# Kernel optimization log

Hardware: AMD Instinct MI355X
Metric: run time of the kernel (lower is better)

## Reference

```python
import jax, jax.numpy as jnp
import numpy as np
from jax import lax

EPS = 1e-4  # BatchNorm eps from the module
K = 3       # kernel_size
PAD = 1     # padding


def setup_inputs() -> dict:
    key = jax.random.key(0)
    k1, k2, k3 = jax.random.split(key, 3)
    N, Cin, H, Wd = 32, 256, 56, 56
    Cout = 256
    x = jax.random.normal(k1, (N, Cin, H, Wd), dtype=jnp.float32)
    gamma = jnp.ones((Cin,), dtype=jnp.float32)
    beta_bn = jnp.zeros((Cin,), dtype=jnp.float32)
    W = jax.random.normal(k2, (Cout, Cin, K, K), dtype=jnp.float32) * 0.05
    b = jax.random.normal(k3, (Cout,), dtype=jnp.float32) * 0.01
    return {"x": x, "gamma": gamma, "beta_bn": beta_bn, "W": W, "b": b}


def _conv(x, w, padding):
    return lax.conv_general_dilated(
        x, w, window_strides=(1, 1),
        padding=[(padding, padding), (padding, padding)],
        dimension_numbers=("NCHW", "OIHW", "NCHW"))


def reference(x, gamma, beta_bn, W, b):
    # BatchNorm2d in training mode: batch statistics over (N, H, W), biased var
    mu = jnp.mean(x, axis=(0, 2, 3), keepdims=True)
    var = jnp.var(x, axis=(0, 2, 3), keepdims=True)
    xn = (x - mu) * lax.rsqrt(var + EPS)
    xn = xn * gamma[None, :, None, None] + beta_bn[None, :, None, None]

    # BinActiv: per-pixel channel-mean of |x|, then sign-binarize
    m = jnp.mean(jnp.abs(xn), axis=1, keepdims=True)  # [N,1,H,W]
    xb = jnp.sign(xn)

    # Binarize weights; alpha = L1 norm per output filter / n
    n = W.shape[1] * W.shape[2] * W.shape[3]
    alpha = jnp.sum(jnp.abs(W), axis=(1, 2, 3)) / n  # [Cout]
    Wb = jnp.sign(W)

    y = _conv(xb, Wb, PAD) + b[None, :, None, None]

    # beta map: box filter (stride 1) over channel-mean magnitudes
    box = jnp.full((1, 1, K, K), 1.0 / (K * K), dtype=x.dtype)
    beta_map = _conv(m, box, PAD)  # [N,1,Ho,Wo]

    out = jax.nn.relu(y * beta_map * alpha[None, :, None, None])
    return out
```

## Files before the change

### kernel.cpp

```cpp
#include <hip/hip_runtime.h>
#include <cstdint>
#include <cstddef>

#define N_    32
#define C_    256
#define H_    56
#define W_    56
#define HW_   (H_ * W_)
#define NHW_  (N_ * HW_)
#define COUT_ 256
#define EPS_  1e-4f
#define PW_   58
#define PIMG_ (PW_ * PW_)

__global__ void k_bn_partial(const float* __restrict__ x,
                             float* __restrict__ ps, float* __restrict__ pq) {
    const int c = blockIdx.x >> 3;
    const int s = blockIdx.x & 7;
    const int t = threadIdx.x;
    float sm = 0.f, sq = 0.f;
    for (int n = s * 4; n < s * 4 + 4; ++n) {
        const float4* p = (const float4*)(x + (size_t)(n * C_ + c) * HW_);
        for (int i = t; i < HW_ / 4; i += 256) {
            float4 v = p[i];
            sm += v.x + v.y + v.z + v.w;
            sq += v.x * v.x + v.y * v.y + v.z * v.z + v.w * v.w;
        }
    }
    __shared__ float ls[256], lq[256];
    ls[t] = sm; lq[t] = sq;
    __syncthreads();
    for (int off = 128; off >= 1; off >>= 1) {
        if (t < off) { ls[t] += ls[t + off]; lq[t] += lq[t + off]; }
        __syncthreads();
    }
    if (t == 0) { ps[s * C_ + c] = ls[0]; pq[s * C_ + c] = lq[0]; }
}

__global__ void k_bn_final(const float* __restrict__ ps, const float* __restrict__ pq,
                           const float* __restrict__ gamma, const float* __restrict__ beta,
                           float* __restrict__ a, float* __restrict__ bb) {
    const int c = threadIdx.x;
    float sm = 0.f, sq = 0.f;
    for (int s = 0; s < 8; ++s) { sm += ps[s * C_ + c]; sq += pq[s * C_ + c]; }
    float mu   = sm * (1.f / NHW_);
    float var  = sq * (1.f / NHW_) - mu * mu;
    float rstd = rsqrtf(var + EPS_);
    float g    = gamma[c] * rstd;
    a[c]  = g;
    bb[c] = beta[c] - mu * g;
}

__global__ void k_wpack(const float* __restrict__ Wt, float* __restrict__ alpha,
                        uint64_t* __restrict__ wbits, int* __restrict__ ctab) {
    const int co = blockIdx.x;
    const int ci = threadIdx.x;
    const int lane = ci & 63, wave = ci >> 6;
    const float* p = Wt + (size_t)(co * C_ + ci) * 9;
    float wv[9];
    float asum = 0.f;
#pragma unroll
    for (int t = 0; t < 9; ++t) { wv[t] = p[t]; asum += fabsf(wv[t]); }
    __shared__ int Pl[9];
    if (ci < 9) Pl[ci] = 0;
    __syncthreads();
#pragma unroll
    for (int t = 0; t < 9; ++t) {
        uint64_t mask = __ballot(wv[t] > 0.f);
        if (lane == 0) {
            wbits[(co * 9 + t) * 4 + wave] = mask;
            atomicAdd(&Pl[t], (int)__popcll(mask));
        }
    }
    __shared__ float red[256];
    red[ci] = asum;
    __syncthreads();
    for (int off = 128; off >= 1; off >>= 1) {
        if (ci < off) red[ci] += red[ci + off];
        __syncthreads();
    }
    if (ci == 0) alpha[co] = red[0] * (1.f / 2304.f);
    if (ci < 9) {
        const int rc = ci / 3, cc = ci % 3;
        unsigned m9 = (rc == 0 ? 0x007u : 0u) | (rc == 2 ? 0x1C0u : 0u)
                    | (cc == 0 ? 0x049u : 0u) | (cc == 2 ? 0x124u : 0u);
        int s = 0;
#pragma unroll
        for (int t = 0; t < 9; ++t)
            if ((m9 >> t) & 1) s += 2 * Pl[t] - 256;
        ctab[ci * 256 + co] = s;
    }
}

__global__ void k_mpack(const float* __restrict__ x, const float* __restrict__ a,
                        const float* __restrict__ bb, uint64_t* __restrict__ xbits,
                        float* __restrict__ m) {
    const int p = blockIdx.x * 256 + threadIdx.x;
    const int wd = blockIdx.y;
    const int n = p / HW_;
    const int hw = p - n * HW_;
    const int h = hw / W_;
    const int w = hw - h * W_;
    const float* xp = x + (size_t)n * C_ * HW_ + (size_t)(wd * 64) * HW_ + hw;
    float macc = 0.f;
    uint64_t bw = 0;
#pragma unroll
    for (int j = 0; j < 64; ++j) {
        const int c = wd * 64 + j;
        float xn = fmaf(xp[(size_t)j * HW_], a[c], bb[c]);
        macc += fabsf(xn);
        bw |= (xn > 0.f) ? (1ull << j) : 0ull;
    }
    xbits[((size_t)n * PIMG_ + (size_t)(h + 1) * PW_ + (w + 1)) * 4 + wd] = bw;
    atomicAdd(&m[p], macc * (1.f / C_));
}

__global__ void k_box(const float* __restrict__ m, float* __restrict__ beta_map) {
    const int idx = blockIdx.x * 256 + threadIdx.x;
    if (idx >= NHW_) return;
    const int w = idx % W_;
    const int h = (idx / W_) % H_;
    const int n = idx / HW_;
    const float* mp = m + (size_t)n * HW_;
    float s = 0.f;
#pragma unroll
    for (int dh = 0; dh < 3; ++dh) {
        int ih = h + dh - 1;
        if (ih < 0 || ih >= H_) continue;
#pragma unroll
        for (int dw = 0; dw < 3; ++dw) {
            int iw = w + dw - 1;
            if (iw < 0 || iw >= W_) continue;
            s += mp[ih * W_ + iw];
        }
    }
    beta_map[idx] = s * (1.f / 9.f);
}

__global__ void __launch_bounds__(256, 3)
k_conv(const uint64_t* __restrict__ xbits, const uint64_t* __restrict__ wbits,
       const int* __restrict__ ctab, const float* __restrict__ beta_map,
       const float* __restrict__ alpha, const float* __restrict__ bias,
       float* __restrict__ out) {
    const int p   = blockIdx.x * 256 + (int)threadIdx.x;
    const int grp = blockIdx.y;
    const int n  = p / HW_;
    const int hw = p - n * HW_;
    const int h  = hw / W_;
    const int w  = hw - h * W_;

    const uint64_t* xb = xbits + ((size_t)n * PIMG_ + (size_t)h * PW_ + w) * 4;
    uint64_t xw[36];
#pragma unroll
    for (int dh = 0; dh < 3; ++dh)
#pragma unroll
        for (int dw = 0; dw < 3; ++dw) {
            const ulonglong2* tp = (const ulonglong2*)(xb + ((size_t)dh * PW_ + dw) * 4);
            ulonglong2 v0 = tp[0];
            ulonglong2 v1 = tp[1];
            xw[(dh * 3 + dw) * 4 + 0] = v0.x;
            xw[(dh * 3 + dw) * 4 + 1] = v0.y;
            xw[(dh * 3 + dw) * 4 + 2] = v1.x;
            xw[(dh * 3 + dw) * 4 + 3] = v1.y;
        }

    const int rowcls = (h == 0) ? 0 : ((h == H_ - 1) ? 2 : 1);
    const int colcls = (w == 0) ? 0 : ((w == W_ - 1) ? 2 : 1);
    const int* crow = ctab + (rowcls * 3 + colcls) * 256 + grp * 64;

    const float bm = beta_map[p];
    float* op = out + (size_t)n * COUT_ * HW_ + (size_t)(grp * 64) * HW_ + hw;

    for (int coi = 0; coi < 64; ++coi) {
        const int co = grp * 64 + coi;
        const uint64_t* wq = wbits + (size_t)co * 36;
        int a0 = 0, a1 = 0, a2 = 0, a3 = 0;
#pragma unroll
        for (int t = 0; t < 9; ++t) {
            a0 += (int)__popcll(xw[t * 4 + 0] ^ wq[t * 4 + 0]);
            a1 += (int)__popcll(xw[t * 4 + 1] ^ wq[t * 4 + 1]);
            a2 += (int)__popcll(xw[t * 4 + 2] ^ wq[t * 4 + 2]);
            a3 += (int)__popcll(xw[t * 4 + 3] ^ wq[t * 4 + 3]);
        }
        const int acc = (a0 + a1) + (a2 + a3);
        const int dot = 2304 - 2 * acc + crow[coi];
        float o = ((float)dot + bias[co]) * bm * alpha[co];
        o = fmaxf(o, 0.f);
        op[(size_t)coi * HW_] = o;
    }
}

extern "C" void kernel_launch(void* const* d_in, const int* in_sizes, int n_in,
                              void* d_out, int out_size, void* d_ws, size_t ws_size,
                              hipStream_t stream) {
    (void)in_sizes; (void)n_in; (void)out_size; (void)ws_size;
    const float* x     = (const float*)d_in[0];
    const float* gamma = (const float*)d_in[1];
    const float* betab = (const float*)d_in[2];
    const float* Wt    = (const float*)d_in[3];
    const float* b     = (const float*)d_in[4];
    float* out = (float*)d_out;

    uint8_t* base = (uint8_t*)d_ws;
    float*    ps       = (float*)(base + 0);
    float*    pq       = (float*)(base + 8192);
    float*    a        = (float*)(base + 16384);
    float*    bb       = (float*)(base + 17408);
    float*    alpha    = (float*)(base + 18432);
    int*      ctab     = (int*)(base + 19456);
    uint64_t* wbits    = (uint64_t*)(base + 28672);
    uint64_t* xbits    = (uint64_t*)(base + 102400);
    float*    m        = (float*)(base + 3547136);
    float*    beta_map = (float*)(base + 3948544);

    k_bn_partial<<<2048, 256, 0, stream>>>(x, ps, pq);
    k_bn_final<<<1, 256, 0, stream>>>(ps, pq, gamma, betab, a, bb);
    k_wpack<<<COUT_, 256, 0, stream>>>(Wt, alpha, wbits, ctab);
    hipMemsetAsync(xbits, 0, (size_t)N_ * PIMG_ * 4 * sizeof(uint64_t), stream);
    hipMemsetAsync(m, 0, (size_t)NHW_ * sizeof(float), stream);
    k_mpack<<<dim3(NHW_ / 256, 4), 256, 0, stream>>>(x, a, bb, xbits, m);
    k_box<<<(NHW_ + 255) / 256, 256, 0, stream>>>(m, beta_map);
    k_conv<<<dim3(NHW_ / 256, 4), 256, 0, stream>>>(xbits, wbits, ctab, beta_map, alpha, b, out);
}
```

Before: 340.4 us.

## Split packed bit planes by channel word and loop conv over words with accumulators

Activation and weight bit masks are re-laid out so each 64-channel word forms its own plane. The conv kernel now loops over the four channel words, loads only 9 words per pass instead of 36, and keeps 64 integer accumulators, one per output channel. This cuts live registers for the input window and raises the launch-bounds occupancy target from 3 to 4. The cost is that weights are re-read in four passes, and the 64 accumulators may create their own register pressure or spill.

```diff
diff --git a/kernel.cpp b/kernel.cpp
--- a/kernel.cpp
+++ b/kernel.cpp
@@ -68,7 +68,7 @@
     for (int t = 0; t < 9; ++t) {
         uint64_t mask = __ballot(wv[t] > 0.f);
         if (lane == 0) {
-            wbits[(co * 9 + t) * 4 + wave] = mask;
+            wbits[((size_t)wave * COUT_ + co) * 9 + t] = mask;
             atomicAdd(&Pl[t], (int)__popcll(mask));
         }
     }
@@ -111,7 +111,7 @@
         macc += fabsf(xn);
         bw |= (xn > 0.f) ? (1ull << j) : 0ull;
     }
-    xbits[((size_t)n * PIMG_ + (size_t)(h + 1) * PW_ + (w + 1)) * 4 + wd] = bw;
+    xbits[((size_t)wd * N_ + n) * PIMG_ + (size_t)(h + 1) * PW_ + (w + 1)] = bw;
     atomicAdd(&m[p], macc * (1.f / C_));
 }
 
@@ -137,7 +137,7 @@
     beta_map[idx] = s * (1.f / 9.f);
 }
 
-__global__ void __launch_bounds__(256, 3)
+__global__ void __launch_bounds__(256, 4)
 k_conv(const uint64_t* __restrict__ xbits, const uint64_t* __restrict__ wbits,
        const int* __restrict__ ctab, const float* __restrict__ beta_map,
        const float* __restrict__ alpha, const float* __restrict__ bias,
@@ -149,41 +149,40 @@
     const int h  = hw / W_;
     const int w  = hw - h * W_;
 
-    const uint64_t* xb = xbits + ((size_t)n * PIMG_ + (size_t)h * PW_ + w) * 4;
-    uint64_t xw[36];
-#pragma unroll
-    for (int dh = 0; dh < 3; ++dh)
-#pragma unroll
-        for (int dw = 0; dw < 3; ++dw) {
-            const ulonglong2* tp = (const ulonglong2*)(xb + ((size_t)dh * PW_ + dw) * 4);
-            ulonglong2 v0 = tp[0];
-            ulonglong2 v1 = tp[1];
-            xw[(dh * 3 + dw) * 4 + 0] = v0.x;
-            xw[(dh * 3 + dw) * 4 + 1] = v0.y;
-            xw[(dh * 3 + dw) * 4 + 2] = v1.x;
-            xw[(dh * 3 + dw) * 4 + 3] = v1.y;
-        }
+    int acc[64];
+#pragma unroll
+    for (int i = 0; i < 64; ++i) acc[i] = 0;
+
+#pragma unroll 1
+    for (int wd = 0; wd < 4; ++wd) {
+        const uint64_t* xp = xbits + ((size_t)wd * N_ + n) * PIMG_ + (size_t)h * PW_ + w;
+        const uint64_t x0 = xp[0],           x1 = xp[1],            x2 = xp[2];
+        const uint64_t x3 = xp[PW_],         x4 = xp[PW_ + 1],      x5 = xp[PW_ + 2];
+        const uint64_t x6 = xp[2 * PW_],     x7 = xp[2 * PW_ + 1],  x8 = xp[2 * PW_ + 2];
+
+        const uint64_t* wq = wbits + ((size_t)wd * COUT_ + grp * 64) * 9;
+#pragma unroll
+        for (int coi = 0; coi < 64; ++coi) {
+            const uint64_t* wr = wq + coi * 9;
+            int s = (int)__popcll(x0 ^ wr[0]) + (int)__popcll(x1 ^ wr[1])
+                  + (int)__popcll(x2 ^ wr[2]) + (int)__popcll(x3 ^ wr[3])
+                  + (int)__popcll(x4 ^ wr[4]) + (int)__popcll(x5 ^ wr[5])
+                  + (int)__popcll(x6 ^ wr[6]) + (int)__popcll(x7 ^ wr[7])
+                  + (int)__popcll(x8 ^ wr[8]);
+            acc[coi] += s;
+        }
+    }
 
     const int rowcls = (h == 0) ? 0 : ((h == H_ - 1) ? 2 : 1);
     const int colcls = (w == 0) ? 0 : ((w == W_ - 1) ? 2 : 1);
     const int* crow = ctab + (rowcls * 3 + colcls) * 256 + grp * 64;
-
     const float bm = beta_map[p];
     float* op = out + (size_t)n * COUT_ * HW_ + (size_t)(grp * 64) * HW_ + hw;
 
+#pragma unroll
     for (int coi = 0; coi < 64; ++coi) {
         const int co = grp * 64 + coi;
-        const uint64_t* wq = wbits + (size_t)co * 36;
-        int a0 = 0, a1 = 0, a2 = 0, a3 = 0;
-#pragma unroll
-        for (int t = 0; t < 9; ++t) {
-            a0 += (int)__popcll(xw[t * 4 + 0] ^ wq[t * 4 + 0]);
-            a1 += (int)__popcll(xw[t * 4 + 1] ^ wq[t * 4 + 1]);
-            a2 += (int)__popcll(xw[t * 4 + 2] ^ wq[t * 4 + 2]);
-            a3 += (int)__popcll(xw[t * 4 + 3] ^ wq[t * 4 + 3]);
-        }
-        const int acc = (a0 + a1) + (a2 + a3);
-        const int dot = 2304 - 2 * acc + crow[coi];
+        const int dot = 2304 - 2 * acc[coi] + crow[coi];
         float o = ((float)dot + bias[co]) * bm * alpha[co];
         o = fmaxf(o, 0.f);
         op[(size_t)coi * HW_] = o;
```

New measurement: 359.1 us. +5.5%, slower.
